# Kernel optimization log

Hardware: AMD Instinct MI355X
Metric: run time of the kernel (lower is better)

The kernel has to match this reference:

```python
import jax, jax.numpy as jnp
import numpy as np

NEG_INF = -1e9  # Keras masked-softmax additive constant
EPS = 1e-6      # LayerNormalization epsilon


def setup_inputs() -> dict:
    key = jax.random.key(0)
    ks = jax.random.split(key, 12)
    B, S, D, H, dk = 4, 2048, 1024, 16, 64
    s = 0.02
    return {
        "x":  jax.random.normal(ks[0], (B, S, D), jnp.float32),
        "Wq": jax.random.normal(ks[1], (D, H, dk), jnp.float32) * s,
        "bq": jnp.zeros((H, dk), jnp.float32),
        "Wk": jax.random.normal(ks[2], (D, H, dk), jnp.float32) * s,
        "bk": jnp.zeros((H, dk), jnp.float32),
        "Wv": jax.random.normal(ks[3], (D, H, dk), jnp.float32) * s,
        "bv": jnp.zeros((H, dk), jnp.float32),
        "Wo": jax.random.normal(ks[4], (H, dk, D), jnp.float32) * s,
        "bo": jnp.zeros((D,), jnp.float32),
        "gamma": jnp.ones((D,), jnp.float32),
        "beta": jnp.zeros((D,), jnp.float32),
    }


def reference(x, Wq, bq, Wk, bk, Wv, bv, Wo, bo, gamma, beta):
    B, S, D = x.shape
    H, dk = Wq.shape[1], Wq.shape[2]
    # per-head projections  [B,S,H,dk]
    q = jnp.einsum("bsd,dhk->bshk", x, Wq) + bq
    k = jnp.einsum("bsd,dhk->bshk", x, Wk) + bk
    v = jnp.einsum("bsd,dhk->bshk", x, Wv) + bv
    # scaled scores  [B,H,Sq,Sk]
    scores = jnp.einsum("bqhk,bshk->bhqs", q, k) / jnp.sqrt(jnp.asarray(dk, x.dtype))
    # causal mask: attend only to positions <= query position
    causal = jnp.tril(jnp.ones((S, S), bool))
    scores = scores + jnp.where(causal, 0.0, NEG_INF).astype(scores.dtype)
    attn = jax.nn.softmax(scores, axis=-1)
    ctx = jnp.einsum("bhqs,bshk->bqhk", attn, v)  # [B,S,H,dk]
    attn_out = jnp.einsum("bqhk,hkd->bqd", ctx, Wo) + bo  # [B,S,D]
    # residual + LayerNorm (dropout is identity at inference)
    y = x + attn_out
    mu = jnp.mean(y, axis=-1, keepdims=True)
    var = jnp.mean(jnp.square(y - mu), axis=-1, keepdims=True)
    return (y - mu) * jax.lax.rsqrt(var + EPS) * gamma + beta
```

## Files before the change

### kernel.cpp

```cpp
#include <hip/hip_runtime.h>


typedef __attribute__((ext_vector_type(8))) short short8;
typedef __attribute__((ext_vector_type(4))) float f32x4;

#define S_LEN 2048
#define NH 16
#define DK 64
#define DMODEL 1024
#define QSCALE 0.18033688011112042f

__device__ inline float fast_exp2(float x) { return __builtin_amdgcn_exp2f(x); }

__device__ inline unsigned short f2bf(float f) {
    unsigned int u = __builtin_bit_cast(unsigned int, f);
    unsigned int r = (u + 0x7fffu + ((u >> 16) & 1u)) >> 16;
    return (unsigned short)r;
}

__device__ inline void gload16(const unsigned short* g, unsigned short* lds) {
    __builtin_amdgcn_global_load_lds(
        (const __attribute__((address_space(1))) void*)g,
        (__attribute__((address_space(3))) void*)lds, 16, 0, 0);
}

__global__ __launch_bounds__(256) void cast_x_kernel(const float* __restrict__ x,
                                                     unsigned short* __restrict__ xb,
                                                     int n4) {
    int i = blockIdx.x * 256 + threadIdx.x;
    if (i >= n4) return;
    float4 v = reinterpret_cast<const float4*>(x)[i];
    ushort4 o;
    o.x = f2bf(v.x); o.y = f2bf(v.y); o.z = f2bf(v.z); o.w = f2bf(v.w);
    reinterpret_cast<ushort4*>(xb)[i] = o;
}

__global__ __launch_bounds__(256) void transpose_cast_kernel(
    const float* __restrict__ s0, const float* __restrict__ s1,
    const float* __restrict__ s2, const float* __restrict__ s3,
    unsigned short* __restrict__ d0, unsigned short* __restrict__ d1,
    unsigned short* __restrict__ d2, unsigned short* __restrict__ d3) {
    int z = blockIdx.z;
    const float* in = z == 0 ? s0 : z == 1 ? s1 : z == 2 ? s2 : s3;
    unsigned short* out = z == 0 ? d0 : z == 1 ? d1 : z == 2 ? d2 : d3;
    __shared__ float t[64][65];
    int i0 = blockIdx.x * 64, j0 = blockIdx.y * 64;
    int tid = threadIdx.x, r = tid >> 4, c4 = (tid & 15) * 4;
    for (int rr = 0; rr < 4; ++rr) {
        float4 v = *reinterpret_cast<const float4*>(&in[(size_t)(i0 + rr * 16 + r) * 1024 + j0 + c4]);
        t[rr * 16 + r][c4 + 0] = v.x; t[rr * 16 + r][c4 + 1] = v.y;
        t[rr * 16 + r][c4 + 2] = v.z; t[rr * 16 + r][c4 + 3] = v.w;
    }
    __syncthreads();
    for (int rr = 0; rr < 4; ++rr) {
        int orow = rr * 16 + r;
        ushort4 o;
        o.x = f2bf(t[c4 + 0][orow]); o.y = f2bf(t[c4 + 1][orow]);
        o.z = f2bf(t[c4 + 2][orow]); o.w = f2bf(t[c4 + 3][orow]);
        *reinterpret_cast<ushort4*>(&out[(size_t)(j0 + orow) * 1024 + i0 + c4]) = o;
    }
}

template <int MODE>
__global__ __launch_bounds__(256) void gemm_bt_kernel(
    const unsigned short* __restrict__ A, const unsigned short* __restrict__ Bt,
    int M, int N, int K,
    unsigned short* __restrict__ qb, unsigned short* __restrict__ kb,
    unsigned short* __restrict__ vbT,
    const float* __restrict__ bq, const float* __restrict__ bk,
    const float* __restrict__ bv,
    const float* __restrict__ xres, const float* __restrict__ bo,
    float* __restrict__ out) {
    __shared__ unsigned short smem[17408];
    unsigned short* Al = smem;
    unsigned short* Bl = smem + 8192;
    unsigned short* Ct = smem;
    int tid = threadIdx.x;
    int m0 = blockIdx.y * 128, n0 = blockIdx.x * 128;
    int w = tid >> 6, l = tid & 63, g = l >> 4, lr = l & 15;
    int wr = (w >> 1) * 64, wc = (w & 1) * 64;
    int srow = tid >> 3, scol = (tid & 7) * 8;
    unsigned short* AlW = Al + w * 512;
    unsigned short* BlW = Bl + w * 512;
    f32x4 acc[4][4];
    for (int i = 0; i < 4; ++i)
        for (int j = 0; j < 4; ++j)
            for (int e = 0; e < 4; ++e) acc[i][j][e] = 0.0f;

    for (int k0 = 0; k0 < K; k0 += 64) {
        const unsigned short* Ap = A + (size_t)(m0 + srow) * K + k0 + scol;
        const unsigned short* Bp = Bt + (size_t)(n0 + srow) * K + k0 + scol;
        for (int i = 0; i < 4; ++i) gload16(Ap + (size_t)i * 32 * K, AlW + i * 2048);
        for (int i = 0; i < 4; ++i) gload16(Bp + (size_t)i * 32 * K, BlW + i * 2048);
        __syncthreads();
        for (int kk = 0; kk < 64; kk += 32) {
            short8 af[4], bf[4];
            for (int mi = 0; mi < 4; ++mi)
                af[mi] = *reinterpret_cast<const short8*>(&Al[(wr + mi * 16 + lr) * 64 + kk + g * 8]);
            for (int ni = 0; ni < 4; ++ni)
                bf[ni] = *reinterpret_cast<const short8*>(&Bl[(wc + ni * 16 + lr) * 64 + kk + g * 8]);
            for (int mi = 0; mi < 4; ++mi)
                for (int ni = 0; ni < 4; ++ni)
                    acc[mi][ni] = __builtin_amdgcn_mfma_f32_16x16x32_bf16(
                        af[mi], bf[ni], acc[mi][ni], 0, 0, 0);
        }
        __syncthreads();
    }

    if (MODE == 0) {
        bool isv = (n0 >= 2048);
        bool isq = (n0 < 1024);
        const float* bias = isq ? bq : (n0 < 2048) ? bk : bv;
        int nb = n0 & 1023;
        for (int mi = 0; mi < 4; ++mi)
            for (int ni = 0; ni < 4; ++ni) {
                int cl = wc + ni * 16 + lr;
                for (int r = 0; r < 4; ++r) {
                    int ml = wr + mi * 16 + g * 4 + r;
                    float vv = acc[mi][ni][r] + bias[nb + cl];
                    if (isq) vv *= QSCALE;
                    unsigned short bfv = f2bf(vv);
                    if (isv) Ct[cl * 136 + ml] = bfv;
                    else     Ct[ml * 136 + cl] = bfv;
                }
            }
        __syncthreads();
        int chunk = tid & 15, rowb = tid >> 4;
        int bb = m0 >> 11, s0 = m0 & 2047;
        for (int it = 0; it < 8; ++it) {
            int rr = it * 16 + rowb;
            short8 vd = *reinterpret_cast<const short8*>(&Ct[rr * 136 + chunk * 8]);
            if (isv) {
                int nn = nb + rr, hh = nn >> 6, kk2 = nn & 63;
                *reinterpret_cast<short8*>(
                    &vbT[(((size_t)bb * NH + hh) * DK + kk2) * S_LEN + s0 + chunk * 8]) = vd;
            } else {
                int nn = nb + chunk * 8, hh = nn >> 6, kk2 = nn & 63;
                unsigned short* dst = isq ? qb : kb;
                *reinterpret_cast<short8*>(
                    &dst[(((size_t)bb * NH + hh) * S_LEN + s0 + rr) * DK + kk2]) = vd;
            }
        }
    } else {
        for (int mi = 0; mi < 4; ++mi)
            for (int ni = 0; ni < 4; ++ni) {
                int col = n0 + wc + ni * 16 + lr;
                for (int r = 0; r < 4; ++r) {
                    int m = m0 + wr + mi * 16 + g * 4 + r;
                    out[(size_t)m * DMODEL + col] =
                        acc[mi][ni][r] + bo[col] + xres[(size_t)m * DMODEL + col];
                }
            }
    }
}

__global__ __launch_bounds__(512) void attn_kernel(const unsigned short* __restrict__ qb,
                                                   const unsigned short* __restrict__ kb,
                                                   const unsigned short* __restrict__ vbT,
                                                   unsigned short* __restrict__ ctx) {
    __shared__ unsigned short Kl[64][72];
    __shared__ unsigned short Vt[64][72];
    __shared__ unsigned short Pl[128][72];
    int j = blockIdx.x;
    int L = ((j & 7) << 7) | (j >> 3);
    int pair = L & 15, h = (L >> 4) & 15, b = L >> 8;
    size_t base = ((size_t)b * NH + h) * S_LEN * DK;
    int tid = threadIdx.x, w = tid >> 6, l = tid & 63, g = l >> 4, lr = l & 15;
    int si = w >> 2, ws = w & 3;
    int myqt = si ? 31 - pair : pair;
    int q0 = myqt * 64;
    int nt = 32 - pair;
    int r8 = tid >> 3, c8 = (tid & 7) * 8;
    int prow = si * 64 + ws * 16;

    uint4 kreg, vreg;
    kreg = *reinterpret_cast<const uint4*>(&kb[base + (size_t)r8 * DK + c8]);
    vreg = *reinterpret_cast<const uint4*>(&vbT[base + (size_t)r8 * S_LEN + c8]);

    short8 qf[2];
    for (int ks = 0; ks < 2; ++ks)
        qf[ks] = *reinterpret_cast<const short8*>(
            &qb[base + (size_t)(q0 + ws * 16 + lr) * DK + ks * 32 + g * 8]);

    f32x4 ctxa[4];
    for (int f = 0; f < 4; ++f)
        for (int e = 0; e < 4; ++e) ctxa[f][e] = 0.0f;
    float m_r[4], lsum[4];
    for (int r = 0; r < 4; ++r) { m_r[r] = -3e38f; lsum[r] = 0.f; }

    for (int t = 0; t < nt; ++t) {
        int kv0 = t * 64;
        __syncthreads();
        *reinterpret_cast<uint4*>(&Kl[r8][c8]) = kreg;
        *reinterpret_cast<uint4*>(&Vt[r8][c8]) = vreg;
        __syncthreads();
        {
            int nkv = (t + 1 < nt) ? kv0 + 64 : 0;
            kreg = *reinterpret_cast<const uint4*>(&kb[base + (size_t)(nkv + r8) * DK + c8]);
            vreg = *reinterpret_cast<const uint4*>(&vbT[base + (size_t)r8 * S_LEN + nkv + c8]);
        }
        if (t > myqt) continue;

        f32x4 sc[4];
        for (int f = 0; f < 4; ++f)
            for (int e = 0; e < 4; ++e) sc[f][e] = 0.0f;
        __builtin_amdgcn_s_setprio(1);
        for (int ks = 0; ks < 2; ++ks)
            for (int f = 0; f < 4; ++f) {
                short8 kf = *reinterpret_cast<const short8*>(&Kl[f * 16 + lr][ks * 32 + g * 8]);
                sc[f] = __builtin_amdgcn_mfma_f32_16x16x32_bf16(qf[ks], kf, sc[f], 0, 0, 0);
            }
        __builtin_amdgcn_s_setprio(0);
        if (t == myqt) {
            for (int f = 0; f < 4; ++f)
                for (int r = 0; r < 4; ++r) {
                    int colg = kv0 + f * 16 + lr;
                    int rowg = q0 + ws * 16 + g * 4 + r;
                    if (colg > rowg) sc[f][r] = -3e38f;
                }
        }
        float tm[4];
        for (int r = 0; r < 4; ++r)
            tm[r] = fmaxf(fmaxf(sc[0][r], sc[1][r]), fmaxf(sc[2][r], sc[3][r]));
        bool ok = tm[0] <= m_r[0] + 8.f && tm[1] <= m_r[1] + 8.f &&
                  tm[2] <= m_r[2] + 8.f && tm[3] <= m_r[3] + 8.f;
        if (!__all((int)ok)) {
            for (int mk = 1; mk < 16; mk <<= 1)
                for (int r = 0; r < 4; ++r) tm[r] = fmaxf(tm[r], __shfl_xor(tm[r], mk));
            for (int r = 0; r < 4; ++r) {
                float mn = fmaxf(m_r[r], tm[r]);
                float al = fast_exp2(m_r[r] - mn);
                m_r[r] = mn;
                lsum[r] *= al;
                for (int f = 0; f < 4; ++f) ctxa[f][r] *= al;
            }
        }
        for (int f = 0; f < 4; ++f)
            for (int r = 0; r < 4; ++r) {
                float p = fast_exp2(sc[f][r] - m_r[r]);
                lsum[r] += p;
                Pl[prow + g * 4 + r][f * 16 + lr] = f2bf(p);
            }
        __builtin_amdgcn_s_setprio(1);
        for (int ks = 0; ks < 2; ++ks) {
            short8 pa = *reinterpret_cast<const short8*>(&Pl[prow + lr][ks * 32 + g * 8]);
            for (int f = 0; f < 4; ++f) {
                short8 vf = *reinterpret_cast<const short8*>(&Vt[f * 16 + lr][ks * 32 + g * 8]);
                ctxa[f] = __builtin_amdgcn_mfma_f32_16x16x32_bf16(pa, vf, ctxa[f], 0, 0, 0);
            }
        }
        __builtin_amdgcn_s_setprio(0);
    }
    for (int mk = 1; mk < 16; mk <<= 1)
        for (int r = 0; r < 4; ++r) lsum[r] += __shfl_xor(lsum[r], mk);
    float inv[4];
    for (int r = 0; r < 4; ++r) inv[r] = 1.0f / lsum[r];
    for (int f = 0; f < 4; ++f)
        for (int r = 0; r < 4; ++r) {
            int s = q0 + ws * 16 + g * 4 + r;
            int d = f * 16 + lr;
            ctx[(((size_t)b * S_LEN + s) * NH + h) * DK + d] = f2bf(ctxa[f][r] * inv[r]);
        }
}

__global__ __launch_bounds__(256) void ln_kernel(float* __restrict__ y,
                                                 const float* __restrict__ gamma,
                                                 const float* __restrict__ beta) {
    int row = blockIdx.x, tid = threadIdx.x;
    float4 v = reinterpret_cast<const float4*>(y + (size_t)row * DMODEL)[tid];
    float s = v.x + v.y + v.z + v.w;
    float q = v.x * v.x + v.y * v.y + v.z * v.z + v.w * v.w;
    for (int off = 32; off >= 1; off >>= 1) {
        s += __shfl_down(s, off);
        q += __shfl_down(q, off);
    }
    __shared__ float ss[4], sq[4];
    int w = tid >> 6, l = tid & 63;
    if (l == 0) { ss[w] = s; sq[w] = q; }
    __syncthreads();
    s = ss[0] + ss[1] + ss[2] + ss[3];
    q = sq[0] + sq[1] + sq[2] + sq[3];
    float mu = s * (1.0f / 1024.0f);
    float var = q * (1.0f / 1024.0f) - mu * mu;
    float inv = rsqrtf(var + 1e-6f);
    float4 g4 = reinterpret_cast<const float4*>(gamma)[tid];
    float4 b4 = reinterpret_cast<const float4*>(beta)[tid];
    float4 o;
    o.x = (v.x - mu) * inv * g4.x + b4.x;
    o.y = (v.y - mu) * inv * g4.y + b4.y;
    o.z = (v.z - mu) * inv * g4.z + b4.z;
    o.w = (v.w - mu) * inv * g4.w + b4.w;
    reinterpret_cast<float4*>(y + (size_t)row * DMODEL)[tid] = o;
}

extern "C" void kernel_launch(void* const* d_in, const int* in_sizes, int n_in,
                              void* d_out, int out_size, void* d_ws, size_t ws_size,
                              hipStream_t stream) {
    const float* x     = (const float*)d_in[0];
    const float* Wq    = (const float*)d_in[1];
    const float* bq    = (const float*)d_in[2];
    const float* Wk    = (const float*)d_in[3];
    const float* bk    = (const float*)d_in[4];
    const float* Wv    = (const float*)d_in[5];
    const float* bv    = (const float*)d_in[6];
    const float* Wo    = (const float*)d_in[7];
    const float* bo    = (const float*)d_in[8];
    const float* gamma = (const float*)d_in[9];
    const float* beta  = (const float*)d_in[10];
    float* out = (float*)d_out;
    char* ws = (char*)d_ws;
    unsigned short* xbf   = (unsigned short*)(ws);
    unsigned short* wqkvT = (unsigned short*)(ws + 16777216);
    unsigned short* woT   = (unsigned short*)(ws + 23068672);
    unsigned short* qbuf  = (unsigned short*)(ws + 25165824);
    unsigned short* kbuf  = (unsigned short*)(ws + 41943040);
    unsigned short* vbufT = (unsigned short*)(ws + 58720256);
    unsigned short* ctx   = xbf;

    cast_x_kernel<<<8192, 256, 0, stream>>>(x, xbf, 2097152);
    dim3 tg(16, 16, 4);
    transpose_cast_kernel<<<tg, 256, 0, stream>>>(Wq, Wk, Wv, Wo, wqkvT,
                                                  wqkvT + 1048576, wqkvT + 2097152, woT);

    dim3 g1(24, 64);
    gemm_bt_kernel<0><<<g1, 256, 0, stream>>>(xbf, wqkvT, 8192, 3072, 1024,
                                              qbuf, kbuf, vbufT, bq, bk, bv,
                                              nullptr, nullptr, nullptr);
    attn_kernel<<<1024, 512, 0, stream>>>(qbuf, kbuf, vbufT, ctx);

    dim3 g2(8, 64);
    gemm_bt_kernel<1><<<g2, 256, 0, stream>>>(ctx, woT, 8192, 1024, 1024,
                                              nullptr, nullptr, nullptr,
                                              nullptr, nullptr, nullptr,
                                              x, bo, out);
    ln_kernel<<<8192, 256, 0, stream>>>(out, gamma, beta);
}
```

Baseline: 322.2 us.

## Keep softmax P in registers via transposed QK^T MFMA; swizzle GEMM block order

The attention kernel now computes S^T by swapping MFMA operands, so each lane holds one query row's scores. P is packed to bf16 in registers and fed straight into the PV MFMA, which removes the LDS round trip through the Pl buffer. The V loads are re-indexed to match the new k ordering, and the row max and sum reductions shrink to two cross-lane shuffles. Separately, the GEMM remaps block IDs so consecutive blocks are spread across 8 XCD groups, aiming for better L2 locality. Risks are correctness of the lane/k permutation mapping and a grid-size assumption that blocks divide evenly by 8.

```diff
diff --git a/kernel.cpp b/kernel.cpp
--- a/kernel.cpp
+++ b/kernel.cpp
@@ -16,6 +16,12 @@
     unsigned int u = __builtin_bit_cast(unsigned int, f);
     unsigned int r = (u + 0x7fffu + ((u >> 16) & 1u)) >> 16;
     return (unsigned short)r;
+}
+
+__device__ inline unsigned int cvt_pk_bf16(float lo, float hi) {
+    unsigned int r;
+    asm("v_cvt_pk_bf16_f32 %0, %1, %2" : "=v"(r) : "v"(lo), "v"(hi));
+    return r;
 }
 
 __device__ inline void gload16(const unsigned short* g, unsigned short* lds) {
@@ -76,7 +82,10 @@
     unsigned short* Bl = smem + 8192;
     unsigned short* Ct = smem;
     int tid = threadIdx.x;
-    int m0 = blockIdx.y * 128, n0 = blockIdx.x * 128;
+    int id = blockIdx.y * gridDim.x + blockIdx.x;
+    int cpx = (gridDim.x * gridDim.y) >> 3;
+    int L = (id & 7) * cpx + (id >> 3);
+    int m0 = (L / gridDim.x) * 128, n0 = (L % gridDim.x) * 128;
     int w = tid >> 6, l = tid & 63, g = l >> 4, lr = l & 15;
     int wr = (w >> 1) * 64, wc = (w & 1) * 64;
     int srow = tid >> 3, scol = (tid & 7) * 8;
@@ -160,7 +169,6 @@
                                                    unsigned short* __restrict__ ctx) {
     __shared__ unsigned short Kl[64][72];
     __shared__ unsigned short Vt[64][72];
-    __shared__ unsigned short Pl[128][72];
     int j = blockIdx.x;
     int L = ((j & 7) << 7) | (j >> 3);
     int pair = L & 15, h = (L >> 4) & 15, b = L >> 8;
@@ -171,7 +179,6 @@
     int q0 = myqt * 64;
     int nt = 32 - pair;
     int r8 = tid >> 3, c8 = (tid & 7) * 8;
-    int prow = si * 64 + ws * 16;
 
     uint4 kreg, vreg;
     kreg = *reinterpret_cast<const uint4*>(&kb[base + (size_t)r8 * DK + c8]);
@@ -185,8 +192,7 @@
     f32x4 ctxa[4];
     for (int f = 0; f < 4; ++f)
         for (int e = 0; e < 4; ++e) ctxa[f][e] = 0.0f;
-    float m_r[4], lsum[4];
-    for (int r = 0; r < 4; ++r) { m_r[r] = -3e38f; lsum[r] = 0.f; }
+    float m_s = -3e38f, lsum = 0.f;
 
     for (int t = 0; t < nt; ++t) {
         int kv0 = t * 64;
@@ -202,64 +208,78 @@
         if (t > myqt) continue;
 
         f32x4 sc[4];
-        for (int f = 0; f < 4; ++f)
-            for (int e = 0; e < 4; ++e) sc[f][e] = 0.0f;
+        for (int fa = 0; fa < 4; ++fa)
+            for (int e = 0; e < 4; ++e) sc[fa][e] = 0.0f;
         __builtin_amdgcn_s_setprio(1);
         for (int ks = 0; ks < 2; ++ks)
-            for (int f = 0; f < 4; ++f) {
-                short8 kf = *reinterpret_cast<const short8*>(&Kl[f * 16 + lr][ks * 32 + g * 8]);
-                sc[f] = __builtin_amdgcn_mfma_f32_16x16x32_bf16(qf[ks], kf, sc[f], 0, 0, 0);
+            for (int fa = 0; fa < 4; ++fa) {
+                short8 kf = *reinterpret_cast<const short8*>(&Kl[fa * 16 + lr][ks * 32 + g * 8]);
+                sc[fa] = __builtin_amdgcn_mfma_f32_16x16x32_bf16(kf, qf[ks], sc[fa], 0, 0, 0);
             }
         __builtin_amdgcn_s_setprio(0);
         if (t == myqt) {
+            int qg = q0 + ws * 16 + lr;
+            for (int fa = 0; fa < 4; ++fa)
+                for (int r = 0; r < 4; ++r)
+                    if (kv0 + fa * 16 + g * 4 + r > qg) sc[fa][r] = -3e38f;
+        }
+        float tm = sc[0][0];
+        for (int fa = 0; fa < 4; ++fa)
+            for (int r = 0; r < 4; ++r) tm = fmaxf(tm, sc[fa][r]);
+        tm = fmaxf(tm, __shfl_xor(tm, 16));
+        tm = fmaxf(tm, __shfl_xor(tm, 32));
+        bool ok = tm <= m_s + 8.f;
+        if (!__all((int)ok)) {
+            float mn = fmaxf(m_s, tm);
+            float al = fast_exp2(m_s - mn);
+            m_s = mn;
+            lsum *= al;
+            float ar[4];
+            for (int r = 0; r < 4; ++r) ar[r] = __shfl(al, g * 4 + r);
             for (int f = 0; f < 4; ++f)
-                for (int r = 0; r < 4; ++r) {
-                    int colg = kv0 + f * 16 + lr;
-                    int rowg = q0 + ws * 16 + g * 4 + r;
-                    if (colg > rowg) sc[f][r] = -3e38f;
-                }
-        }
-        float tm[4];
-        for (int r = 0; r < 4; ++r)
-            tm[r] = fmaxf(fmaxf(sc[0][r], sc[1][r]), fmaxf(sc[2][r], sc[3][r]));
-        bool ok = tm[0] <= m_r[0] + 8.f && tm[1] <= m_r[1] + 8.f &&
-                  tm[2] <= m_r[2] + 8.f && tm[3] <= m_r[3] + 8.f;
-        if (!__all((int)ok)) {
-            for (int mk = 1; mk < 16; mk <<= 1)
-                for (int r = 0; r < 4; ++r) tm[r] = fmaxf(tm[r], __shfl_xor(tm[r], mk));
+                for (int r = 0; r < 4; ++r) ctxa[f][r] *= ar[r];
+        }
+        float p[4][4];
+        float ls = 0.f;
+        for (int fa = 0; fa < 4; ++fa)
             for (int r = 0; r < 4; ++r) {
-                float mn = fmaxf(m_r[r], tm[r]);
-                float al = fast_exp2(m_r[r] - mn);
-                m_r[r] = mn;
-                lsum[r] *= al;
-                for (int f = 0; f < 4; ++f) ctxa[f][r] *= al;
-            }
-        }
-        for (int f = 0; f < 4; ++f)
-            for (int r = 0; r < 4; ++r) {
-                float p = fast_exp2(sc[f][r] - m_r[r]);
-                lsum[r] += p;
-                Pl[prow + g * 4 + r][f * 16 + lr] = f2bf(p);
-            }
+                p[fa][r] = fast_exp2(sc[fa][r] - m_s);
+                ls += p[fa][r];
+            }
+        lsum += ls;
+        unsigned int pk[4][2];
+        for (int fa = 0; fa < 4; ++fa) {
+            pk[fa][0] = cvt_pk_bf16(p[fa][0], p[fa][1]);
+            pk[fa][1] = cvt_pk_bf16(p[fa][2], p[fa][3]);
+        }
+        uint4 pa0u = {pk[0][0], pk[0][1], pk[1][0], pk[1][1]};
+        uint4 pa1u = {pk[2][0], pk[2][1], pk[3][0], pk[3][1]};
+        short8 pa0 = __builtin_bit_cast(short8, pa0u);
+        short8 pa1 = __builtin_bit_cast(short8, pa1u);
         __builtin_amdgcn_s_setprio(1);
         for (int ks = 0; ks < 2; ++ks) {
-            short8 pa = *reinterpret_cast<const short8*>(&Pl[prow + lr][ks * 32 + g * 8]);
+            short8 pa = ks ? pa1 : pa0;
             for (int f = 0; f < 4; ++f) {
-                short8 vf = *reinterpret_cast<const short8*>(&Vt[f * 16 + lr][ks * 32 + g * 8]);
+                const unsigned short* vrow = &Vt[f * 16 + lr][0];
+                uint2 lo = *reinterpret_cast<const uint2*>(&vrow[ks * 32 + 4 * g]);
+                uint2 hi = *reinterpret_cast<const uint2*>(&vrow[ks * 32 + 16 + 4 * g]);
+                uint4 vfu = {lo.x, lo.y, hi.x, hi.y};
+                short8 vf = __builtin_bit_cast(short8, vfu);
                 ctxa[f] = __builtin_amdgcn_mfma_f32_16x16x32_bf16(pa, vf, ctxa[f], 0, 0, 0);
             }
         }
         __builtin_amdgcn_s_setprio(0);
     }
-    for (int mk = 1; mk < 16; mk <<= 1)
-        for (int r = 0; r < 4; ++r) lsum[r] += __shfl_xor(lsum[r], mk);
-    float inv[4];
-    for (int r = 0; r < 4; ++r) inv[r] = 1.0f / lsum[r];
+    lsum += __shfl_xor(lsum, 16);
+    lsum += __shfl_xor(lsum, 32);
+    float rl = 1.0f / lsum;
+    float inv_l[4];
+    for (int r = 0; r < 4; ++r) inv_l[r] = __shfl(rl, g * 4 + r);
     for (int f = 0; f < 4; ++f)
         for (int r = 0; r < 4; ++r) {
             int s = q0 + ws * 16 + g * 4 + r;
             int d = f * 16 + lr;
-            ctx[(((size_t)b * S_LEN + s) * NH + h) * DK + d] = f2bf(ctxa[f][r] * inv[r]);
+            ctx[(((size_t)b * S_LEN + s) * NH + h) * DK + d] = f2bf(ctxa[f][r] * inv_l[r]);
         }
 }
 
```

New measurement: 317.3 us. No clear change (-1.5%).
